# Kernel tuning notes

Measured on AMD Instinct MI355X. Metric: run time of the kernel, lower is better.

The kernel has to match this reference:

```python
import jax, jax.numpy as jnp
import numpy as np

EPS = 1e-6  # added only where the 2-way softmax prob is exactly zero (matches torch code)

def setup_inputs() -> dict:
    key = jax.random.key(0)
    k1, k2 = jax.random.split(key)
    B, C = 65536, 1000  # nClass = 1000, input has C+1 logits
    input = jax.random.normal(k1, (B, C + 1), dtype=jnp.float32)
    target = jax.random.randint(k2, (B,), 0, C)  # unused in the math, shape-only
    return {"input": input, "target": target}

def reference(input, target):
    B = input.shape[0]
    logits = input[:, :-1]            # [B, C] class logits
    extra = input[:, -1:]             # [B, 1] shared extra logit
    prob = jax.nn.softmax(logits, axis=1)               # [B, C]
    # 2-way softmax([input[:,i], input[:,-1]])[-1] == sigmoid(extra - logits[:,i])
    pc = jax.nn.sigmoid(extra - logits)                  # [B, C] prob of extra class
    pc_adj = jnp.where(pc == 0, pc + EPS, pc)            # torch adds 1e-6 only where exactly 0
    # sum over classes of per-class batch means == total sum / B
    loss = -(prob * jnp.log(pc_adj)).sum() / B
    return loss
```

## Files before the change

### kernel.cpp

```cpp
#include <hip/hip_runtime.h>
#include <math.h>

#define ROWS 65536
#define COLS 1000
#define STRIDE 1001
#define K1_BLOCKS 2048
#define WAVES_PER_BLOCK 4
#define EPSV 1e-6f

__global__ __launch_bounds__(256) void row_loss_kernel(
    const float* __restrict__ in, float* __restrict__ partial) {
    const int lane  = threadIdx.x & 63;
    const int wave  = threadIdx.x >> 6;
    const int gwave = blockIdx.x * WAVES_PER_BLOCK + wave;
    const int nwaves = gridDim.x * WAVES_PER_BLOCK;

    float wsum = 0.0f;
    for (int row = gwave; row < ROWS; row += nwaves) {
        const float* rp = in + (size_t)row * STRIDE;

        float l[16];
        #pragma unroll
        for (int k = 0; k < 16; ++k) {
            int c = lane + 64 * k;
            l[k] = (c < COLS) ? rp[c] : -INFINITY;
        }
        float extra = rp[COLS];

        float m = l[0];
        #pragma unroll
        for (int k = 1; k < 16; ++k) m = fmaxf(m, l[k]);
        #pragma unroll
        for (int off = 32; off > 0; off >>= 1) m = fmaxf(m, __shfl_xor(m, off));

        float e[16];
        float se = 0.0f;
        #pragma unroll
        for (int k = 0; k < 16; ++k) {
            int c = lane + 64 * k;
            float v = (c < COLS) ? __expf(l[k] - m) : 0.0f;
            e[k] = v;
            se += v;
        }
        #pragma unroll
        for (int off = 32; off > 0; off >>= 1) se += __shfl_xor(se, off);
        float rdenom = 1.0f / se;

        float t = 0.0f;
        #pragma unroll
        for (int k = 0; k < 16; ++k) {
            int c = lane + 64 * k;
            if (c < COLS) {
                float p = e[k] * rdenom;
                float x = extra - l[k];
                float s = __builtin_amdgcn_rcpf(1.0f + __expf(-x));
                if (s == 0.0f) s = EPSV;
                t += p * __logf(s);
            }
        }
        #pragma unroll
        for (int off = 32; off > 0; off >>= 1) t += __shfl_xor(t, off);
        wsum += t;
    }

    __shared__ float sdata[WAVES_PER_BLOCK];
    if (lane == 0) sdata[wave] = wsum;
    __syncthreads();
    if (threadIdx.x == 0) {
        float b = 0.0f;
        #pragma unroll
        for (int w = 0; w < WAVES_PER_BLOCK; ++w) b += sdata[w];
        partial[blockIdx.x] = b;
    }
}

__global__ __launch_bounds__(256) void final_reduce(
    const float* __restrict__ partial, float* __restrict__ out) {
    float s = 0.0f;
    for (int i = threadIdx.x; i < K1_BLOCKS; i += 256) s += partial[i];
    #pragma unroll
    for (int off = 32; off > 0; off >>= 1) s += __shfl_xor(s, off);
    __shared__ float sdata[4];
    const int lane = threadIdx.x & 63, wave = threadIdx.x >> 6;
    if (lane == 0) sdata[wave] = s;
    __syncthreads();
    if (threadIdx.x == 0) {
        float tot = sdata[0] + sdata[1] + sdata[2] + sdata[3];
        out[0] = -tot / (float)ROWS;
    }
}

extern "C" void kernel_launch(void* const* d_in, const int* in_sizes, int n_in,
                              void* d_out, int out_size, void* d_ws, size_t ws_size,
                              hipStream_t stream) {
    const float* in = (const float*)d_in[0];
    float* partial = (float*)d_ws;
    row_loss_kernel<<<K1_BLOCKS, 256, 0, stream>>>(in, partial);
    final_reduce<<<1, 256, 0, stream>>>(partial, (float*)d_out);
}
```

Before: 357.8 us.

## Vectorize row loads with aligned float4 and simplify per-element log-sigmoid math

Each row is now read as aligned float4 vectors with a per-row shift, and out-of-range columns are masked to -inf, replacing scalar strided loads. The loss term is rewritten algebraically: log(sigmoid(extra-l)) = -log(1 + e*exp(m-extra)), so each element needs one exp-reuse, one fma and one log. Normalization by the softmax denominator is applied once per row rather than per element. This trades the exact zero-probability epsilon handling for an overflow check against infinity, which may differ numerically in edge cases. The aligned loads also read a few bytes past row bounds into neighboring rows, which are then masked.

```diff
diff --git a/kernel.cpp b/kernel.cpp
--- a/kernel.cpp
+++ b/kernel.cpp
@@ -4,9 +4,10 @@
 #define ROWS 65536
 #define COLS 1000
 #define STRIDE 1001
+#define ROWBYTES 4004
 #define K1_BLOCKS 2048
 #define WAVES_PER_BLOCK 4
-#define EPSV 1e-6f
+#define NLOGEPS 13.815510558f
 
 __global__ __launch_bounds__(256) void row_loss_kernel(
     const float* __restrict__ in, float* __restrict__ partial) {
@@ -14,18 +15,42 @@
     const int wave  = threadIdx.x >> 6;
     const int gwave = blockIdx.x * WAVES_PER_BLOCK + wave;
     const int nwaves = gridDim.x * WAVES_PER_BLOCK;
+    const char* inb = (const char*)in;
 
     float wsum = 0.0f;
     for (int row = gwave; row < ROWS; row += nwaves) {
-        const float* rp = in + (size_t)row * STRIDE;
+        const size_t base  = (size_t)row * ROWBYTES;
+        const size_t abase = base & ~(size_t)15;
+        const int shift    = (int)((base & 15) >> 2);
+        const float4* rp4  = (const float4*)(inb + abase);
+        const float*  rp   = (const float*)(inb + base);
+
+        float4 vv[4];
+        vv[0] = rp4[lane];
+        vv[1] = rp4[lane + 64];
+        vv[2] = rp4[lane + 128];
+        vv[3] = make_float4(0.f, 0.f, 0.f, 0.f);
+        if (lane <= 58) vv[3] = rp4[lane + 192];
+        float extra = rp[COLS];
 
         float l[16];
         #pragma unroll
-        for (int k = 0; k < 16; ++k) {
-            int c = lane + 64 * k;
-            l[k] = (c < COLS) ? rp[c] : -INFINITY;
+        for (int k = 0; k < 4; ++k) {
+            l[4*k + 0] = vv[k].x;
+            l[4*k + 1] = vv[k].y;
+            l[4*k + 2] = vv[k].z;
+            l[4*k + 3] = vv[k].w;
         }
-        float extra = rp[COLS];
+
+        const int cbase = 4 * lane - shift;
+        #pragma unroll
+        for (int k = 0; k < 4; ++k) {
+            #pragma unroll
+            for (int j = 0; j < 4; ++j) {
+                int c = cbase + 256 * k + j;
+                if ((unsigned)c >= (unsigned)COLS) l[4*k + j] = -INFINITY;
+            }
+        }
 
         float m = l[0];
         #pragma unroll
@@ -37,30 +62,26 @@
         float se = 0.0f;
         #pragma unroll
         for (int k = 0; k < 16; ++k) {
-            int c = lane + 64 * k;
-            float v = (c < COLS) ? __expf(l[k] - m) : 0.0f;
+            float v = __expf(l[k] - m);
             e[k] = v;
             se += v;
         }
         #pragma unroll
         for (int off = 32; off > 0; off >>= 1) se += __shfl_xor(se, off);
-        float rdenom = 1.0f / se;
 
-        float t = 0.0f;
+        const float K = __expf(m - extra);
+        float acc = 0.0f;
         #pragma unroll
         for (int k = 0; k < 16; ++k) {
-            int c = lane + 64 * k;
-            if (c < COLS) {
-                float p = e[k] * rdenom;
-                float x = extra - l[k];
-                float s = __builtin_amdgcn_rcpf(1.0f + __expf(-x));
-                if (s == 0.0f) s = EPSV;
-                t += p * __logf(s);
-            }
+            float u = fmaf(e[k], K, 1.0f);
+            float lg = __logf(u);
+            if (u == INFINITY) lg = NLOGEPS;
+            acc = fmaf(e[k], lg, acc);
         }
         #pragma unroll
-        for (int off = 32; off > 0; off >>= 1) t += __shfl_xor(t, off);
-        wsum += t;
+        for (int off = 32; off > 0; off >>= 1) acc += __shfl_xor(acc, off);
+
+        wsum -= acc / se;
     }
 
     __shared__ float sdata[WAVES_PER_BLOCK];
```

Measured after the change: 356.2 us. Within noise of the previous version (-0.5%).
